# Kernel tuning notes

Measured on AMD Instinct MI355X. Metric: run time of the kernel, lower is better.

## Reference

```python
import jax, jax.numpy as jnp
import numpy as np
import math

B, S_TGT, S_SRC, D, H, FF = 4, 2048, 2048, 512, 8, 2048
DK = D // H
EPS = 1e-6


def layernorm(x, gamma, mu):
    # torch: gamma*(x-mean)/(std+eps)+mu with unbiased std (ddof=1), eps OUTSIDE sqrt
    mean = jnp.mean(x, axis=-1, keepdims=True)
    std = jnp.std(x, axis=-1, keepdims=True, ddof=1)
    return gamma * (x - mean) / (std + EPS) + mu


def mha(q, k, v, wq, wk, wv, wo, bo, mask):
    # q:[B,Sq,D] k,v:[B,Sk,D]; weights [D,D] (applied as x@W)
    Bq, Sq, _ = q.shape
    Sk = k.shape[1]
    Q = (q @ wq).reshape(Bq, Sq, H, DK).transpose(0, 2, 1, 3)  # [B,H,Sq,dk]
    K = (k @ wk).reshape(Bq, Sk, H, DK).transpose(0, 2, 1, 3)
    V = (v @ wv).reshape(Bq, Sk, H, DK).transpose(0, 2, 1, 3)
    scores = jnp.einsum('bhqd,bhkd->bhqk', Q, K) / math.sqrt(DK)
    scores = jnp.where(mask == 0, -1e9, scores)
    attn = jax.nn.softmax(scores, axis=-1)
    out = jnp.einsum('bhqk,bhkd->bhqd', attn, V)  # [B,H,Sq,dk]
    out = out.transpose(0, 2, 1, 3).reshape(Bq, Sq, D)
    return out @ wo + bo


def setup_inputs() -> dict:
    key = jax.random.key(0)
    ks = jax.random.split(key, 20)
    sc = 0.02
    inp = {
        'x': jax.random.normal(ks[0], (B, S_TGT, D), jnp.float32),
        'encoder_output': jax.random.normal(ks[1], (B, S_SRC, D), jnp.float32),
        'src_mask': jnp.ones((1, 1, 1, S_SRC), jnp.int32),
        'tgt_mask': jnp.tril(jnp.ones((S_TGT, S_TGT), jnp.int32))[None, None],
        # self-attention params
        'sa_wq': jax.random.normal(ks[2], (D, D)) * sc,
        'sa_wk': jax.random.normal(ks[3], (D, D)) * sc,
        'sa_wv': jax.random.normal(ks[4], (D, D)) * sc,
        'sa_wo': jax.random.normal(ks[5], (D, D)) * sc,
        'sa_bo': jnp.zeros((D,), jnp.float32),
        # cross-attention params
        'ca_wq': jax.random.normal(ks[6], (D, D)) * sc,
        'ca_wk': jax.random.normal(ks[7], (D, D)) * sc,
        'ca_wv': jax.random.normal(ks[8], (D, D)) * sc,
        'ca_wo': jax.random.normal(ks[9], (D, D)) * sc,
        'ca_bo': jnp.zeros((D,), jnp.float32),
        # feed-forward params
        'ff_w1': jax.random.normal(ks[10], (D, FF)) * sc,
        'ff_b1': jnp.zeros((FF,), jnp.float32),
        'ff_w2': jax.random.normal(ks[11], (FF, D)) * sc,
        'ff_b2': jnp.zeros((D,), jnp.float32),
        # layernorm params (3 residual connections)
        'ln0_g': jnp.ones((D,), jnp.float32), 'ln0_b': jnp.zeros((D,), jnp.float32),
        'ln1_g': jnp.ones((D,), jnp.float32), 'ln1_b': jnp.zeros((D,), jnp.float32),
        'ln2_g': jnp.ones((D,), jnp.float32), 'ln2_b': jnp.zeros((D,), jnp.float32),
    }
    return inp


def reference(x, encoder_output, src_mask, tgt_mask,
              sa_wq, sa_wk, sa_wv, sa_wo, sa_bo,
              ca_wq, ca_wk, ca_wv, ca_wo, ca_bo,
              ff_w1, ff_b1, ff_w2, ff_b2,
              ln0_g, ln0_b, ln1_g, ln1_b, ln2_g, ln2_b):
    # pre-LN residual blocks; dropout in eval mode (identity)
    h = layernorm(x, ln0_g, ln0_b)
    x = x + mha(h, h, h, sa_wq, sa_wk, sa_wv, sa_wo, sa_bo, tgt_mask)
    h = layernorm(x, ln1_g, ln1_b)
    x = x + mha(h, encoder_output, encoder_output, ca_wq, ca_wk, ca_wv, ca_wo, ca_bo, src_mask)
    h = layernorm(x, ln2_g, ln2_b)
    ff = jax.nn.relu(h @ ff_w1 + ff_b1) @ ff_w2 + ff_b2
    return x + ff
```

## Files before the change

### kernel.cpp

```cpp
#include <hip/hip_runtime.h>
#include <cstdint>

typedef short s8v __attribute__((ext_vector_type(8)));
typedef short s4v __attribute__((ext_vector_type(4)));
typedef float f4v __attribute__((ext_vector_type(4)));
typedef unsigned int u32;

#define DEV static __device__ __forceinline__

#if __has_builtin(__builtin_amdgcn_exp2f)
#define EXP2(x) __builtin_amdgcn_exp2f(x)
#else
#define EXP2(x) __expf((x) * 0.69314718056f)
#endif

DEV unsigned short f2bf(float f) {
  u32 u = __builtin_bit_cast(u32, f);
  u += 0x7FFF + ((u >> 16) & 1);
  return (unsigned short)(u >> 16);
}

DEV void gload16(const void* g, void* l) {
  __builtin_amdgcn_global_load_lds(
      (const __attribute__((address_space(1))) u32*)g,
      (__attribute__((address_space(3))) u32*)l, 16, 0, 0);
}

struct TransArgs {
  const float* in[10];
  unsigned short* out[10];
};

__global__ __launch_bounds__(256) void trans_all_kernel(TransArgs ta) {
  int id = blockIdx.x;
  int wi, t, K, N, tx, ty;
  if (id < 2048) {
    wi = id >> 8; t = id & 255; K = 512; N = 512; tx = t & 15; ty = t >> 4;
  } else if (id < 3072) {
    wi = 8; t = id - 2048; K = 512; N = 2048; tx = t & 63; ty = t >> 6;
  } else {
    wi = 9; t = id - 3072; K = 2048; N = 512; tx = t & 15; ty = t >> 4;
  }
  const float* in = ta.in[wi];
  unsigned short* out = ta.out[wi];
  __shared__ float tile[32][33];
  int lx = threadIdx.x & 31, ly = threadIdx.x >> 5;
  int bn = tx * 32, bk = ty * 32;
#pragma unroll
  for (int i = 0; i < 32; i += 8)
    tile[ly + i][lx] = in[(size_t)(bk + ly + i) * N + bn + lx];
  __syncthreads();
#pragma unroll
  for (int i = 0; i < 32; i += 8)
    out[(size_t)(bn + ly + i) * K + bk + lx] = f2bf(tile[lx][ly + i]);
}

__global__ __launch_bounds__(256) void cast_kernel(
    const float* __restrict__ in, unsigned short* __restrict__ out, int n8) {
  int i = blockIdx.x * 256 + threadIdx.x;
  if (i >= n8) return;
  const float4* p = (const float4*)(in + (size_t)i * 8);
  float4 a = p[0], b = p[1];
  float va[8] = {a.x, a.y, a.z, a.w, b.x, b.y, b.z, b.w};
  s8v o;
#pragma unroll
  for (int j = 0; j < 8; j++) o[j] = (short)f2bf(va[j]);
  *(s8v*)(out + (size_t)i * 8) = o;
}

__global__ __launch_bounds__(256) void ln_kernel(
    const float* __restrict__ x, const float* __restrict__ g,
    const float* __restrict__ bt, unsigned short* __restrict__ out) {
  int row = blockIdx.x * 4 + (threadIdx.x >> 6);
  int lane = threadIdx.x & 63;
  const float* xr = x + (size_t)row * 512 + lane * 8;
  float4 v0 = *(const float4*)xr;
  float4 v1 = *(const float4*)(xr + 4);
  float va[8] = {v0.x, v0.y, v0.z, v0.w, v1.x, v1.y, v1.z, v1.w};
  float s = 0.f, s2 = 0.f;
#pragma unroll
  for (int j = 0; j < 8; j++) { s += va[j]; s2 += va[j] * va[j]; }
#pragma unroll
  for (int off = 1; off < 64; off <<= 1) {
    s += __shfl_xor(s, off);
    s2 += __shfl_xor(s2, off);
  }
  float mean = s * (1.f / 512.f);
  float var = (s2 - 512.f * mean * mean) * (1.f / 511.f);
  var = fmaxf(var, 0.f);
  float inv = 1.f / (sqrtf(var) + 1e-6f);
  const float* gp = g + lane * 8;
  const float* bp = bt + lane * 8;
  float4 g0 = *(const float4*)gp, g1 = *(const float4*)(gp + 4);
  float4 b0 = *(const float4*)bp, b1 = *(const float4*)(bp + 4);
  float ga[8] = {g0.x, g0.y, g0.z, g0.w, g1.x, g1.y, g1.z, g1.w};
  float ba[8] = {b0.x, b0.y, b0.z, b0.w, b1.x, b1.y, b1.z, b1.w};
  s8v o;
#pragma unroll
  for (int j = 0; j < 8; j++)
    o[j] = (short)f2bf(ga[j] * (va[j] - mean) * inv + ba[j]);
  *(s8v*)(out + (size_t)row * 512 + lane * 8) = o;
}

#define EPI_QKV3 0
#define EPI_Q 1
#define EPI_KV2 2
#define EPI_BIAS_RES 3
#define EPI_RELU 4

#define QSCALE 0.18033688f

template <int EPI, int BN>
__global__ __launch_bounds__(256, 3) void gemm_kernel(
    const unsigned short* __restrict__ A, const unsigned short* __restrict__ Bt,
    const float* __restrict__ bias, const float* __restrict__ res,
    void* __restrict__ out0, void* __restrict__ out1, void* __restrict__ out2,
    int M, int N, int K) {
  __shared__ alignas(16) unsigned short sA[2][128 * 32];
  __shared__ alignas(16) unsigned short sB[2][BN * 32];
  constexpr int NC = BN / 32;
  int tid = threadIdx.x;
  int w = tid >> 6, lane = tid & 63;
  int wm = w >> 1, wn = w & 1;
  int quad = lane >> 4, l15 = lane & 15;

  int lin = blockIdx.x + gridDim.x * blockIdx.y;
  int xcd = lin & 7, j = lin >> 3;
  int bmi = xcd * 8 + (j & 7);
  int bni = j >> 3;
  int bm = bmi * 128, bn = bni * BN;

  int r0 = lane >> 2, c0 = (lane & 3) * 8;
  const unsigned short* gA0 = A + (size_t)(bm + w * 16 + r0) * K + c0;
  const unsigned short* gA1 = gA0 + (size_t)64 * K;
  const unsigned short* gB0 = Bt + (size_t)(bn + w * 16 + r0) * K + c0;
  const unsigned short* gB1 = gB0 + (size_t)64 * K;

  auto prefetch = [&](int k0, int buf) {
    gload16(gA0 + k0, &sA[buf][w * 512]);
    gload16(gA1 + k0, &sA[buf][(w + 4) * 512]);
    gload16(gB0 + k0, &sB[buf][w * 512]);
    if (BN == 128) gload16(gB1 + k0, &sB[buf][(w + 4) * 512]);
  };

  f4v acc[4][NC];
#pragma unroll
  for (int r = 0; r < 4; r++)
#pragma unroll
    for (int c = 0; c < NC; c++) acc[r][c] = {0.f, 0.f, 0.f, 0.f};

  prefetch(0, 0);
  int nk = K >> 5;
  for (int it = 0; it < nk; it++) {
    int buf = it & 1;
    __syncthreads();
    if (it + 1 < nk) prefetch((it + 1) << 5, buf ^ 1);
    s8v af[4], bf[NC];
#pragma unroll
    for (int r = 0; r < 4; r++)
      af[r] = *(const s8v*)&sA[buf][(wm * 64 + r * 16 + l15) * 32 + quad * 8];
#pragma unroll
    for (int c = 0; c < NC; c++)
      bf[c] = *(const s8v*)&sB[buf][(wn * (BN / 2) + c * 16 + l15) * 32 + quad * 8];
#pragma unroll
    for (int r = 0; r < 4; r++)
#pragma unroll
      for (int c = 0; c < NC; c++)
        acc[r][c] = __builtin_amdgcn_mfma_f32_16x16x32_bf16(af[r], bf[c], acc[r][c], 0, 0, 0);
  }

  constexpr int BP = 512 / BN;
  int route = 0;
  if (EPI == EPI_QKV3) route = bni / BP;
  if (EPI == EPI_KV2) route = 1 + bni / BP;
#pragma unroll
  for (int r = 0; r < 4; r++) {
#pragma unroll
    for (int c = 0; c < NC; c++) {
#pragma unroll
      for (int i = 0; i < 4; i++) {
        int row = bm + wm * 64 + r * 16 + quad * 4 + i;
        int col = bn + wn * (BN / 2) + c * 16 + l15;
        float v = acc[r][c][i];
        if (EPI == EPI_BIAS_RES) {
          float* o = (float*)out0;
          o[(size_t)row * N + col] = v + bias[col] + res[(size_t)row * N + col];
        } else if (EPI == EPI_RELU) {
          unsigned short* o = (unsigned short*)out0;
          o[(size_t)row * N + col] = f2bf(fmaxf(v + bias[col], 0.f));
        } else {
          int colq = col & 511;
          int b = row >> 11, s = row & 2047, h = colq >> 6, dk = colq & 63;
          if (route == 0) {
            unsigned short* o = (unsigned short*)out0;
            o[(((size_t)(b * 8 + h) * 2048) + s) * 64 + dk] = f2bf(v * QSCALE);
          } else if (route == 1) {
            unsigned short* o = (unsigned short*)out1;
            o[(((size_t)(b * 8 + h) * 2048) + s) * 64 + dk] = f2bf(v);
          } else {
            unsigned short* o = (unsigned short*)out2;
            o[(((size_t)(b * 8 + h) * 64) + dk) * 2048 + s] = f2bf(v);
          }
        }
      }
    }
  }
}

template <int CAUSAL>
__global__ __launch_bounds__(256, 2) void attn_kernel(
    const unsigned short* __restrict__ Q, const unsigned short* __restrict__ Kk,
    const unsigned short* __restrict__ Vt,
    unsigned short* __restrict__ out) {
  const int S = 2048;
  __shared__ alignas(16) unsigned short sK[2][64 * 64];
  __shared__ alignas(16) unsigned short sV[2][64 * 64];
  __shared__ alignas(16) unsigned short sO[128 * 68];
  int bh = blockIdx.x;
  int qt = CAUSAL ? ((int)gridDim.y - 1 - blockIdx.y) : blockIdx.y;
  int b = bh >> 3, h = bh & 7;
  int tid = threadIdx.x;
  int w = tid >> 6, lane = tid & 63;
  int quad = lane >> 4, l15 = lane & 15;

  const unsigned short* Qp = Q + (size_t)bh * S * 64;
  const unsigned short* Kp = Kk + (size_t)bh * S * 64;
  const unsigned short* Vp = Vt + (size_t)bh * 64 * S;

  s8v bq[2][2];
#pragma unroll
  for (int qb = 0; qb < 2; qb++) {
    const unsigned short* qr =
        Qp + (size_t)(qt * 128 + w * 32 + qb * 16 + l15) * 64 + quad * 8;
    bq[qb][0] = *(const s8v*)qr;
    bq[qb][1] = *(const s8v*)(qr + 32);
  }

  int rowA = ((l15 >> 2) * 8) + (l15 & 3);
  int koff[2][2][2];
#pragma unroll
  for (int win = 0; win < 2; win++)
#pragma unroll
    for (int half = 0; half < 2; half++) {
      int row = win * 32 + half * 4 + rowA;
      int h7 = (row & 7) ^ (((row >> 3) & 1) << 2);
      koff[win][half][0] = row * 64 + ((quad ^ h7) << 3);
      koff[win][half][1] = row * 64 + (((4 + quad) ^ h7) << 3);
    }
  int voff[4][2];
#pragma unroll
  for (int c2 = 0; c2 < 4; c2++) {
    int row = c2 * 16 + l15;
    int h7 = (row & 7) ^ (((row >> 3) & 1) << 2);
#pragma unroll
    for (int win = 0; win < 2; win++)
      voff[c2][win] = row * 64 + ((((win * 4) + quad) ^ h7) << 3);
  }
  int st_row[2], st_lds[2], st_cc[2];
#pragma unroll
  for (int c = 0; c < 2; c++) {
    int row = c * 32 + (tid >> 3), cc = tid & 7;
    int slot = cc ^ (row & 7) ^ (((row >> 3) & 1) << 2);
    st_row[c] = row;
    st_cc[c] = cc;
    st_lds[c] = row * 64 + slot * 8;
  }

  float l_lane[2] = {0.f, 0.f};
  f4v oacc[2][4];
#pragma unroll
  for (int qb = 0; qb < 2; qb++)
#pragma unroll
    for (int c2 = 0; c2 < 4; c2++) oacc[qb][c2] = {0.f, 0.f, 0.f, 0.f};

  int ntiles = CAUSAL ? (2 * qt + 2) : (S / 64);

  s8v kreg[2], vreg[2];
  auto load_t = [&](int t) {
    int kb = t * 64;
#pragma unroll
    for (int c = 0; c < 2; c++) {
      kreg[c] = *(const s8v*)(Kp + (size_t)(kb + st_row[c]) * 64 + st_cc[c] * 8);
      vreg[c] = *(const s8v*)(Vp + (size_t)st_row[c] * S + kb + st_cc[c] * 8);
    }
  };
  auto write_t = [&](int buf) {
#pragma unroll
    for (int c = 0; c < 2; c++) {
      *(s8v*)&sK[buf][st_lds[c]] = kreg[c];
      *(s8v*)&sV[buf][st_lds[c]] = vreg[c];
    }
  };

  load_t(0);
  write_t(0);

  for (int t = 0; t < ntiles; t++) {
    int buf = t & 1;
    __syncthreads();
    if (t + 1 < ntiles) load_t(t + 1);

    f4v sacc[2][2][2];
#pragma unroll
    for (int qb = 0; qb < 2; qb++)
#pragma unroll
      for (int win = 0; win < 2; win++)
#pragma unroll
        for (int half = 0; half < 2; half++) sacc[qb][win][half] = {0.f, 0.f, 0.f, 0.f};
#pragma unroll
    for (int win = 0; win < 2; win++)
#pragma unroll
      for (int half = 0; half < 2; half++) {
        s8v a0 = *(const s8v*)&sK[buf][koff[win][half][0]];
        s8v a1 = *(const s8v*)&sK[buf][koff[win][half][1]];
#pragma unroll
        for (int qb = 0; qb < 2; qb++) {
          sacc[qb][win][half] =
              __builtin_amdgcn_mfma_f32_16x16x32_bf16(a0, bq[qb][0], sacc[qb][win][half], 0, 0, 0);
          sacc[qb][win][half] =
              __builtin_amdgcn_mfma_f32_16x16x32_bf16(a1, bq[qb][1], sacc[qb][win][half], 0, 0, 0);
        }
      }

    if (CAUSAL && t >= 2 * qt) {
      int toff = (t - 2 * qt) * 64;
#pragma unroll
      for (int qb = 0; qb < 2; qb++) {
        int qloc = w * 32 + qb * 16 + l15;
#pragma unroll
        for (int win = 0; win < 2; win++)
#pragma unroll
          for (int half = 0; half < 2; half++)
#pragma unroll
            for (int i = 0; i < 4; i++)
              if (toff + win * 32 + quad * 8 + half * 4 + i > qloc)
                sacc[qb][win][half][i] = -1e9f;
      }
    }

    s8v bp[2][2];
#pragma unroll
    for (int qb = 0; qb < 2; qb++)
#pragma unroll
      for (int win = 0; win < 2; win++) {
        float p[8];
#pragma unroll
        for (int half = 0; half < 2; half++)
#pragma unroll
          for (int i = 0; i < 4; i++) {
            float e = EXP2(sacc[qb][win][half][i]);
            p[half * 4 + i] = e;
            l_lane[qb] += e;
          }
        int4 pk;
#pragma unroll
        for (int jj = 0; jj < 4; jj++)
          pk[jj] = (int)__builtin_amdgcn_perm(
              __builtin_bit_cast(u32, p[2 * jj + 1]),
              __builtin_bit_cast(u32, p[2 * jj]), 0x07060302u);
        bp[qb][win] = __builtin_bit_cast(s8v, pk);
      }

#pragma unroll
    for (int c2 = 0; c2 < 4; c2++)
#pragma unroll
      for (int win = 0; win < 2; win++) {
        s8v av = *(const s8v*)&sV[buf][voff[c2][win]];
#pragma unroll
        for (int qb = 0; qb < 2; qb++)
          oacc[qb][c2] =
              __builtin_amdgcn_mfma_f32_16x16x32_bf16(av, bp[qb][win], oacc[qb][c2], 0, 0, 0);
      }

    if (t + 1 < ntiles) write_t(buf ^ 1);
  }

#pragma unroll
  for (int qb = 0; qb < 2; qb++) {
    float l = l_lane[qb];
    l += __shfl_xor(l, 16);
    l += __shfl_xor(l, 32);
    float inv = 1.f / l;
#pragma unroll
    for (int c2 = 0; c2 < 4; c2++) {
      s4v o;
#pragma unroll
      for (int i = 0; i < 4; i++) o[i] = (short)f2bf(oacc[qb][c2][i] * inv);
      *(s4v*)&sO[(w * 32 + qb * 16 + l15) * 68 + c2 * 16 + quad * 4] = o;
    }
  }
  __syncthreads();
#pragma unroll
  for (int c = 0; c < 4; c++) {
    int idx = c * 256 + tid;
    int r = idx >> 3, ch = idx & 7;
    s8v v = *(const s8v*)&sO[r * 68 + ch * 8];
    *(s8v*)(out + ((size_t)(b * S + qt * 128 + r) * 512) + h * 64 + ch * 8) = v;
  }
}

extern "C" void kernel_launch(void* const* d_in, const int* in_sizes, int n_in,
                              void* d_out, int out_size, void* d_ws, size_t ws_size,
                              hipStream_t stream) {
  const float* x = (const float*)d_in[0];
  const float* enc = (const float*)d_in[1];
  const float* sa_wq = (const float*)d_in[4];
  const float* sa_wk = (const float*)d_in[5];
  const float* sa_wv = (const float*)d_in[6];
  const float* sa_wo = (const float*)d_in[7];
  const float* sa_bo = (const float*)d_in[8];
  const float* ca_wq = (const float*)d_in[9];
  const float* ca_wk = (const float*)d_in[10];
  const float* ca_wv = (const float*)d_in[11];
  const float* ca_wo = (const float*)d_in[12];
  const float* ca_bo = (const float*)d_in[13];
  const float* ff_w1 = (const float*)d_in[14];
  const float* ff_b1 = (const float*)d_in[15];
  const float* ff_w2 = (const float*)d_in[16];
  const float* ff_b2 = (const float*)d_in[17];
  const float* ln0_g = (const float*)d_in[18];
  const float* ln0_b = (const float*)d_in[19];
  const float* ln1_g = (const float*)d_in[20];
  const float* ln1_b = (const float*)d_in[21];
  const float* ln2_g = (const float*)d_in[22];
  const float* ln2_b = (const float*)d_in[23];
  float* out = (float*)d_out;

  const int M = 8192;

  size_t off = 0;
  auto carve = [&](size_t bytes) -> void* {
    void* r = (char*)d_ws + off;
    off += (bytes + 255) & ~(size_t)255;
    return r;
  };
  unsigned short* swqT = (unsigned short*)carve(512 * 512 * 2);
  unsigned short* swkT = (unsigned short*)carve(512 * 512 * 2);
  unsigned short* swvT = (unsigned short*)carve(512 * 512 * 2);
  unsigned short* swoT = (unsigned short*)carve(512 * 512 * 2);
  unsigned short* cwqT = (unsigned short*)carve(512 * 512 * 2);
  unsigned short* cwkT = (unsigned short*)carve(512 * 512 * 2);
  unsigned short* cwvT = (unsigned short*)carve(512 * 512 * 2);
  unsigned short* cwoT = (unsigned short*)carve(512 * 512 * 2);
  unsigned short* w1T = (unsigned short*)carve((size_t)2048 * 512 * 2);
  unsigned short* w2T = (unsigned short*)carve((size_t)512 * 2048 * 2);
  unsigned short* enc_bf = (unsigned short*)carve((size_t)M * 512 * 2);
  unsigned short* h_bf = (unsigned short*)carve((size_t)M * 512 * 2);
  unsigned short* Qb = (unsigned short*)carve((size_t)M * 512 * 2);
  unsigned short* Kb = (unsigned short*)carve((size_t)M * 512 * 2);
  unsigned short* Vtb = (unsigned short*)carve((size_t)M * 512 * 2);
  unsigned short* attn_bf = (unsigned short*)carve((size_t)M * 512 * 2);
  float* x1 = (float*)carve((size_t)M * 512 * 4);
  unsigned short* f1 = (unsigned short*)carve((size_t)M * 2048 * 2);

  dim3 blk(256);

  TransArgs ta;
  ta.in[0] = sa_wq; ta.out[0] = swqT;
  ta.in[1] = sa_wk; ta.out[1] = swkT;
  ta.in[2] = sa_wv; ta.out[2] = swvT;
  ta.in[3] = sa_wo; ta.out[3] = swoT;
  ta.in[4] = ca_wq; ta.out[4] = cwqT;
  ta.in[5] = ca_wk; ta.out[5] = cwkT;
  ta.in[6] = ca_wv; ta.out[6] = cwvT;
  ta.in[7] = ca_wo; ta.out[7] = cwoT;
  ta.in[8] = ff_w1; ta.out[8] = w1T;
  ta.in[9] = ff_w2; ta.out[9] = w2T;
  trans_all_kernel<<<dim3(4096), blk, 0, stream>>>(ta);
  cast_kernel<<<dim3(M * 512 / 8 / 256), blk, 0, stream>>>(enc, enc_bf, M * 512 / 8);

  dim3 gProj(8, 64);
  dim3 gQKV(12, 64);
  dim3 gKV(16, 64);
  dim3 gFF1(16, 64);
  dim3 gAttn(32, 16);
  dim3 gLN(M / 4);

  ln_kernel<<<gLN, blk, 0, stream>>>(x, ln0_g, ln0_b, h_bf);
  gemm_kernel<EPI_QKV3, 128><<<gQKV, blk, 0, stream>>>(h_bf, swqT, nullptr, nullptr, Qb, Kb, Vtb, M, 1536, 512);
  attn_kernel<1><<<gAttn, blk, 0, stream>>>(Qb, Kb, Vtb, attn_bf);
  gemm_kernel<EPI_BIAS_RES, 64><<<gProj, blk, 0, stream>>>(attn_bf, swoT, sa_bo, x, x1, nullptr, nullptr, M, 512, 512);

  ln_kernel<<<gLN, blk, 0, stream>>>(x1, ln1_g, ln1_b, h_bf);
  gemm_kernel<EPI_Q, 64><<<gProj, blk, 0, stream>>>(h_bf, cwqT, nullptr, nullptr, Qb, nullptr, nullptr, M, 512, 512);
  gemm_kernel<EPI_KV2, 64><<<gKV, blk, 0, stream>>>(enc_bf, cwkT, nullptr, nullptr, nullptr, Kb, Vtb, M, 1024, 512);
  attn_kernel<0><<<gAttn, blk, 0, stream>>>(Qb, Kb, Vtb, attn_bf);
  gemm_kernel<EPI_BIAS_RES, 64><<<gProj, blk, 0, stream>>>(attn_bf, cwoT, ca_bo, x1, x1, nullptr, nullptr, M, 512, 512);

  ln_kernel<<<gLN, blk, 0, stream>>>(x1, ln2_g, ln2_b, h_bf);
  gemm_kernel<EPI_RELU, 128><<<gFF1, blk, 0, stream>>>(h_bf, w1T, ff_b1, nullptr, f1, nullptr, nullptr, M, 2048, 512);
  gemm_kernel<EPI_BIAS_RES, 64><<<gProj, blk, 0, stream>>>(f1, w2T, ff_b2, x1, out, nullptr, nullptr, M, 512, 2048);
}
```

Baseline: 371.4 us.

## Parameterize GEMM K-tile depth, reorder causal tile schedule, interleave attention P·V

Adds a BK template parameter to the GEMM, giving a generalized cooperative global-to-LDS load, an inner k-substep loop, and BK=64 for the BN=64 GEMMs so each barrier covers twice as much MFMA work. The causal attention grid now launches the eight heaviest query tiles first, then the light ones in ascending order, to balance work across CUs. The softmax-to-PV loop is restructured per window so the packed probabilities for one window are consumed before the next is computed, which may lower register pressure. The larger LDS tiles in BK=64 kernels could reduce occupancy.

```diff
diff --git a/kernel.cpp b/kernel.cpp
--- a/kernel.cpp
+++ b/kernel.cpp
@@ -110,15 +110,18 @@
 
 #define QSCALE 0.18033688f
 
-template <int EPI, int BN>
+template <int EPI, int BN, int BK>
 __global__ __launch_bounds__(256, 3) void gemm_kernel(
     const unsigned short* __restrict__ A, const unsigned short* __restrict__ Bt,
     const float* __restrict__ bias, const float* __restrict__ res,
     void* __restrict__ out0, void* __restrict__ out1, void* __restrict__ out2,
     int M, int N, int K) {
-  __shared__ alignas(16) unsigned short sA[2][128 * 32];
-  __shared__ alignas(16) unsigned short sB[2][BN * 32];
+  __shared__ alignas(16) unsigned short sA[2][128 * BK];
+  __shared__ alignas(16) unsigned short sB[2][BN * BK];
   constexpr int NC = BN / 32;
+  constexpr int NKK = BK / 32;
+  constexpr int ASTEP = 128 * BK / 2048;
+  constexpr int BSTEP = BN * BK / 2048;
   int tid = threadIdx.x;
   int w = tid >> 6, lane = tid & 63;
   int wm = w >> 1, wn = w & 1;
@@ -130,17 +133,20 @@
   int bni = j >> 3;
   int bm = bmi * 128, bn = bni * BN;
 
-  int r0 = lane >> 2, c0 = (lane & 3) * 8;
-  const unsigned short* gA0 = A + (size_t)(bm + w * 16 + r0) * K + c0;
-  const unsigned short* gA1 = gA0 + (size_t)64 * K;
-  const unsigned short* gB0 = Bt + (size_t)(bn + w * 16 + r0) * K + c0;
-  const unsigned short* gB1 = gB0 + (size_t)64 * K;
+  constexpr int LPR = BK / 8;
+  int srow = (tid / LPR);
+  int scol = (tid % LPR) * 8;
+  const unsigned short* gA = A + (size_t)(bm + srow) * K + scol;
+  const unsigned short* gB = Bt + (size_t)(bn + srow) * K + scol;
+  constexpr int RSTEP = 2048 / BK;
 
   auto prefetch = [&](int k0, int buf) {
-    gload16(gA0 + k0, &sA[buf][w * 512]);
-    gload16(gA1 + k0, &sA[buf][(w + 4) * 512]);
-    gload16(gB0 + k0, &sB[buf][w * 512]);
-    if (BN == 128) gload16(gB1 + k0, &sB[buf][(w + 4) * 512]);
+#pragma unroll
+    for (int s = 0; s < ASTEP; s++)
+      gload16(gA + (size_t)s * RSTEP * K + k0, &sA[buf][s * 2048 + tid * 8]);
+#pragma unroll
+    for (int s = 0; s < BSTEP; s++)
+      gload16(gB + (size_t)s * RSTEP * K + k0, &sB[buf][s * 2048 + tid * 8]);
   };
 
   f4v acc[4][NC];
@@ -150,23 +156,26 @@
     for (int c = 0; c < NC; c++) acc[r][c] = {0.f, 0.f, 0.f, 0.f};
 
   prefetch(0, 0);
-  int nk = K >> 5;
+  int nk = K / BK;
   for (int it = 0; it < nk; it++) {
     int buf = it & 1;
     __syncthreads();
-    if (it + 1 < nk) prefetch((it + 1) << 5, buf ^ 1);
-    s8v af[4], bf[NC];
-#pragma unroll
-    for (int r = 0; r < 4; r++)
-      af[r] = *(const s8v*)&sA[buf][(wm * 64 + r * 16 + l15) * 32 + quad * 8];
-#pragma unroll
-    for (int c = 0; c < NC; c++)
-      bf[c] = *(const s8v*)&sB[buf][(wn * (BN / 2) + c * 16 + l15) * 32 + quad * 8];
-#pragma unroll
-    for (int r = 0; r < 4; r++)
+    if (it + 1 < nk) prefetch((it + 1) * BK, buf ^ 1);
+#pragma unroll
+    for (int kk = 0; kk < NKK; kk++) {
+      s8v af[4], bf[NC];
+#pragma unroll
+      for (int r = 0; r < 4; r++)
+        af[r] = *(const s8v*)&sA[buf][(wm * 64 + r * 16 + l15) * BK + kk * 32 + quad * 8];
 #pragma unroll
       for (int c = 0; c < NC; c++)
-        acc[r][c] = __builtin_amdgcn_mfma_f32_16x16x32_bf16(af[r], bf[c], acc[r][c], 0, 0, 0);
+        bf[c] = *(const s8v*)&sB[buf][(wn * (BN / 2) + c * 16 + l15) * BK + kk * 32 + quad * 8];
+#pragma unroll
+      for (int r = 0; r < 4; r++)
+#pragma unroll
+        for (int c = 0; c < NC; c++)
+          acc[r][c] = __builtin_amdgcn_mfma_f32_16x16x32_bf16(af[r], bf[c], acc[r][c], 0, 0, 0);
+    }
   }
 
   constexpr int BP = 512 / BN;
@@ -217,7 +226,8 @@
   __shared__ alignas(16) unsigned short sV[2][64 * 64];
   __shared__ alignas(16) unsigned short sO[128 * 68];
   int bh = blockIdx.x;
-  int qt = CAUSAL ? ((int)gridDim.y - 1 - blockIdx.y) : blockIdx.y;
+  int y = blockIdx.y;
+  int qt = CAUSAL ? ((y < 8) ? (15 - y) : (y - 8)) : y;
   int b = bh >> 3, h = bh & 7;
   int tid = threadIdx.x;
   int w = tid >> 6, lane = tid & 63;
@@ -338,11 +348,11 @@
       }
     }
 
-    s8v bp[2][2];
-#pragma unroll
-    for (int qb = 0; qb < 2; qb++)
-#pragma unroll
-      for (int win = 0; win < 2; win++) {
+#pragma unroll
+    for (int win = 0; win < 2; win++) {
+      s8v bp[2];
+#pragma unroll
+      for (int qb = 0; qb < 2; qb++) {
         float p[8];
 #pragma unroll
         for (int half = 0; half < 2; half++)
@@ -358,19 +368,17 @@
           pk[jj] = (int)__builtin_amdgcn_perm(
               __builtin_bit_cast(u32, p[2 * jj + 1]),
               __builtin_bit_cast(u32, p[2 * jj]), 0x07060302u);
-        bp[qb][win] = __builtin_bit_cast(s8v, pk);
+        bp[qb] = __builtin_bit_cast(s8v, pk);
       }
-
-#pragma unroll
-    for (int c2 = 0; c2 < 4; c2++)
-#pragma unroll
-      for (int win = 0; win < 2; win++) {
+#pragma unroll
+      for (int c2 = 0; c2 < 4; c2++) {
         s8v av = *(const s8v*)&sV[buf][voff[c2][win]];
 #pragma unroll
         for (int qb = 0; qb < 2; qb++)
           oacc[qb][c2] =
-              __builtin_amdgcn_mfma_f32_16x16x32_bf16(av, bp[qb][win], oacc[qb][c2], 0, 0, 0);
+              __builtin_amdgcn_mfma_f32_16x16x32_bf16(av, bp[qb], oacc[qb][c2], 0, 0, 0);
       }
+    }
 
     if (t + 1 < ntiles) write_t(buf ^ 1);
   }
@@ -477,17 +485,17 @@
   dim3 gLN(M / 4);
 
   ln_kernel<<<gLN, blk, 0, stream>>>(x, ln0_g, ln0_b, h_bf);
-  gemm_kernel<EPI_QKV3, 128><<<gQKV, blk, 0, stream>>>(h_bf, swqT, nullptr, nullptr, Qb, Kb, Vtb, M, 1536, 512);
+  gemm_kernel<EPI_QKV3, 128, 32><<<gQKV, blk, 0, stream>>>(h_bf, swqT, nullptr, nullptr, Qb, Kb, Vtb, M, 1536, 512);
   attn_kernel<1><<<gAttn, blk, 0, stream>>>(Qb, Kb, Vtb, attn_bf);
-  gemm_kernel<EPI_BIAS_RES, 64><<<gProj, blk, 0, stream>>>(attn_bf, swoT, sa_bo, x, x1, nullptr, nullptr, M, 512, 512);
+  gemm_kernel<EPI_BIAS_RES, 64, 64><<<gProj, blk, 0, stream>>>(attn_bf, swoT, sa_bo, x, x1, nullptr, nullptr, M, 512, 512);
 
   ln_kernel<<<gLN, blk, 0, stream>>>(x1, ln1_g, ln1_b, h_bf);
-  gemm_kernel<EPI_Q, 64><<<gProj, blk, 0, stream>>>(h_bf, cwqT, nullptr, nullptr, Qb, nullptr, nullptr, M, 512, 512);
-  gemm_kernel<EPI_KV2, 64><<<gKV, blk, 0, stream>>>(enc_bf, cwkT, nullptr, nullptr, nullptr, Kb, Vtb, M, 1024, 512);
+  gemm_kernel<EPI_Q, 64, 64><<<gProj, blk, 0, stream>>>(h_bf, cwqT, nullptr, nullptr, Qb, nullptr, nullptr, M, 512, 512);
+  gemm_kernel<EPI_KV2, 64, 64><<<gKV, blk, 0, stream>>>(enc_bf, cwkT, nullptr, nullptr, nullptr, Kb, Vtb, M, 1024, 512);
   attn_kernel<0><<<gAttn, blk, 0, stream>>>(Qb, Kb, Vtb, attn_bf);
-  gemm_kernel<EPI_BIAS_RES, 64><<<gProj, blk, 0, stream>>>(attn_bf, cwoT, ca_bo, x1, x1, nullptr, nullptr, M, 512, 512);
+  gemm_kernel<EPI_BIAS_RES, 64, 64><<<gProj, blk, 0, stream>>>(attn_bf, cwoT, ca_bo, x1, x1, nullptr, nullptr, M, 512, 512);
 
   ln_kernel<<<gLN, blk, 0, stream>>>(x1, ln2_g, ln2_b, h_bf);
-  gemm_kernel<EPI_RELU, 128><<<gFF1, blk, 0, stream>>>(h_bf, w1T, ff_b1, nullptr, f1, nullptr, nullptr, M, 2048, 512);
-  gemm_kernel<EPI_BIAS_RES, 64><<<gProj, blk, 0, stream>>>(f1, w2T, ff_b2, x1, out, nullptr, nullptr, M, 512, 2048);
-}
+  gemm_kernel<EPI_RELU, 128, 32><<<gFF1, blk, 0, stream>>>(h_bf, w1T, ff_b1, nullptr, f1, nullptr, nullptr, M, 2048, 512);
+  gemm_kernel<EPI_BIAS_RES, 64, 64><<<gProj, blk, 0, stream>>>(f1, w2T, ff_b2, x1, out, nullptr, nullptr, M, 512, 2048);
+}
```

New measurement: 388.7 us. 4.7% more time.
